# Optimization experiments

Hardware: AMD Instinct MI355X
Metric: run time of the kernel (lower is better)

Reference implementation:

```python
import jax, jax.numpy as jnp
import numpy as np
from jax import lax

NI, NH, NO = 128, 64, 128
PERIODS = np.array([1, 2, 4, 8, 16, 32, 64, 128], dtype=np.int32)
NCLOCKS = len(PERIODS)
K = NCLOCKS * NH  # total hidden size = 512
T, B = 512, 256


def _glorotize(W):
    W = W * np.sqrt(6.0)
    W = W / np.sqrt(np.sum(W.shape))
    return W


def _recurrent_mask():
    # block upper-triangular: row block r can read hidden blocks r..NCLOCKS-1
    rows = []
    for c in range(NCLOCKS, 0, -1):
        zero = np.zeros((NH, NH * (NCLOCKS - c)))
        one = np.ones((NH, NH * c))
        rows.append(np.concatenate([zero, one], axis=1))
    return np.concatenate(rows, axis=0)


def setup_inputs() -> dict:
    key = jax.random.key(0)
    kx = jax.random.fold_in(key, 0)
    rng = np.random.default_rng(0)
    X = jax.random.normal(kx, (T, B, NI), dtype=jnp.float32)
    Wi = _glorotize(rng.standard_normal((K, NI + 1)))
    Wh = rng.standard_normal((K, K + 1))
    U, _, _ = np.linalg.svd(Wh[:, :-1])
    Wh[:, :-1] = U * _recurrent_mask()
    Wo = _glorotize(rng.standard_normal((NO, K + 1)))
    return {
        "X": X,
        "Wi": jnp.asarray(Wi, jnp.float32),
        "Wh": jnp.asarray(Wh, jnp.float32),
        "Wo": jnp.asarray(Wo, jnp.float32),
    }


def reference(X, Wi, Wh, Wo):
    # X: (T, B, NI). Original code treats trailing axis as batch after transpose.
    periods = jnp.repeat(jnp.asarray(PERIODS), NH)               # (K,)
    active = ((jnp.arange(T)[:, None] % periods[None, :]) == 0)  # (T, K)
    active = active.astype(X.dtype)

    Xt = jnp.swapaxes(X, 1, 2)                                   # (T, NI, B)
    Wi_w, Wi_b = Wi[:, :-1], Wi[:, -1:]                          # (K,NI),(K,1)
    Wh_w, Wh_b = Wh[:, :-1], Wh[:, -1:]                          # (K,K),(K,1)
    Wo_w, Wo_b = Wo[:, :-1], Wo[:, -1:]                          # (NO,K),(NO,1)

    def step(H_prev, inp):
        x, a = inp                                               # (NI,B),(K,)
        i_h = Wi_w @ x + Wi_b                                    # (K,B)
        H_new = jnp.tanh(i_h + Wh_w @ H_prev + Wh_b)             # (K,B)
        a = a[:, None]
        H = a * H_new + (1.0 - a) * H_prev                       # clock gating
        y = jnp.tanh(Wo_w @ H + Wo_b)                            # (NO,B)
        return H, y

    H0 = jnp.zeros((K, B), dtype=X.dtype)
    H, Ys = lax.scan(step, H0, (Xt, active))                     # Ys: (T,NO,B)
    return jnp.swapaxes(Ys, 1, 2), H                             # (T,B,NO),(K,B)
```

## Files before the change

kernel.cpp:

```cpp
#include <hip/hip_runtime.h>


typedef unsigned int  u32;
typedef unsigned short u16;
typedef _Float16 f16;
typedef f16   f16x2 __attribute__((ext_vector_type(2)));
typedef f16   f16x8 __attribute__((ext_vector_type(8)));
typedef float f32x4 __attribute__((ext_vector_type(4)));

#define TT   512
#define BB   256
#define NI_  128
#define NO_  128

#define WIP_N   32768
#define WHRP_N  49152
#define WHLP_N  30720
#define WOA_N   32768
#define ICOMP_PER_B 65280
#define IOFF(j_) (65536 - (65536 >> (j_)))

__device__ __forceinline__ u32 pk2(float a, float b){
  f16x2 v; v.x=(f16)a; v.y=(f16)b; return __builtin_bit_cast(u32, v);
}
__device__ __forceinline__ float tanh_fast(float x){
  float e = __expf(2.0f*x);
  return 1.0f - 2.0f/(e + 1.0f);
}
__device__ __forceinline__ float dot2(u32 a, u32 b, float c){
#if __has_builtin(__builtin_amdgcn_fdot2)
  return __builtin_amdgcn_fdot2(__builtin_bit_cast(f16x2,a), __builtin_bit_cast(f16x2,b), c, false);
#else
  f16x2 x = __builtin_bit_cast(f16x2,a), y = __builtin_bit_cast(f16x2,b);
  c = fmaf((float)x.x,(float)y.x,c); c = fmaf((float)x.y,(float)y.y,c); return c;
#endif
}
__device__ __forceinline__ float f16at_rt(uint4 v, int i){
  u32 w = (i&4) ? ((i&2)? v.w : v.z) : ((i&2)? v.y : v.x);
  w = (i&1) ? (w>>16) : (w & 0xffffu);
  return (float)__builtin_bit_cast(f16, (u16)w);
}
__device__ __forceinline__ float f16at2(uint2 v, int i){
  u32 w = (i&2) ? v.y : v.x;
  w = (i&1) ? (w>>16) : (w & 0xffffu);
  return (float)__builtin_bit_cast(f16, (u16)w);
}
__device__ __forceinline__ float f16at1(u32 v, int i){
  u32 w = i ? (v>>16) : (v & 0xffffu);
  return (float)__builtin_bit_cast(f16, (u16)w);
}

#define BAR()   asm volatile("s_waitcnt lgkmcnt(0)\n\ts_barrier" ::: "memory")
#define LGKMW() do{ asm volatile("s_waitcnt lgkmcnt(0)" ::: "memory"); \
                    __builtin_amdgcn_sched_barrier(0); }while(0)

__global__ __launch_bounds__(256) void cw_prep(
    const float* __restrict__ Wi, const float* __restrict__ Wh, const float* __restrict__ Wo,
    u32* __restrict__ WiP, u32* __restrict__ WhrP, u32* __restrict__ WhlP, u32* __restrict__ WoAu,
    float* __restrict__ cb, float* __restrict__ wob)
{
  const int NTOT = WIP_N + WHRP_N + WHLP_N + WOA_N + 512 + 128;
  for (int idx = blockIdx.x*blockDim.x + threadIdx.x; idx < NTOT; idx += (int)(gridDim.x*blockDim.x)){
    if (idx < WIP_N){
      int r  = idx >> 6;
      int c2 = idx & 63;
      WiP[idx] = pk2(Wi[r*129 + 2*c2], Wi[r*129 + 2*c2 + 1]);
    } else if (idx < WIP_N + WHRP_N){
      int q32 = idx - WIP_N;
      int slot = q32 >> 11, rr = (q32 >> 5) & 63, c4 = q32 & 31;
      int jj = slot / 3, dq = slot % 3, qq = jj + dq;
      u32 v = 0u;
      if (qq <= 7){
        int row = 64*jj + rr;
        v = pk2(Wh[row*513 + 64*qq + 2*c4], Wh[row*513 + 64*qq + 2*c4 + 1]);
      }
      WhrP[q32] = v;
    } else if (idx < WIP_N + WHRP_N + WHLP_N){
      int q32 = idx - WIP_N - WHRP_N;
      int slot = q32 >> 11, rr = (q32 >> 5) & 63, pos = (q32 >> 2) & 7, e = q32 & 3;
      int jj, qq;
      if      (slot <  5){ jj = 0; qq = slot + 3; }
      else if (slot <  9){ jj = 1; qq = slot - 1; }
      else if (slot < 12){ jj = 2; qq = slot - 4; }
      else if (slot < 14){ jj = 3; qq = slot - 6; }
      else               { jj = 4; qq = 7; }
      int i  = pos ^ (rr & 7);
      int cp = i*4 + e;
      int row = 64*jj + rr;
      WhlP[q32] = pk2(Wh[row*513 + 64*qq + 2*cp], Wh[row*513 + 64*qq + 2*cp + 1]);
    } else if (idx < WIP_N + WHRP_N + WHLP_N + WOA_N){
      int q32 = idx - WIP_N - WHRP_N - WHLP_N;
      int o = q32 >> 8, kp = q32 & 255;
      WoAu[q32] = pk2(Wo[o*513 + 2*kp], Wo[o*513 + 2*kp + 1]);
    } else if (idx < WIP_N + WHRP_N + WHLP_N + WOA_N + 512){
      int r = idx - WIP_N - WHRP_N - WHLP_N - WOA_N;
      cb[r] = Wh[r*513 + 512] + Wi[r*129 + 128];
    } else {
      int o = idx - WIP_N - WHRP_N - WHLP_N - WOA_N - 512;
      wob[o] = Wo[o*513 + 512];
    }
  }
}

__global__ __launch_bounds__(256) void cw_igemm(
    const float* __restrict__ X, const u32* __restrict__ WiP, f16* __restrict__ Icomp)
{
  const int tid = threadIdx.x;
  const int l = tid & 63, w = tid >> 6;
  const int bid = blockIdx.x;
  const int b = bid / 19, sub = bid % 19;
  int j, m0;
  if      (sub <  8){ j = 0; m0 = sub*64; }
  else if (sub < 12){ j = 1; m0 = (sub-8)*64; }
  else if (sub < 14){ j = 2; m0 = (sub-12)*64; }
  else if (sub ==14){ j = 3; m0 = 0; }
  else              { j = sub-11; m0 = 0; }
  const int Nj = 512 >> j;
  const int mt = m0 + w*16;
  const int la = l & 15, lb = l >> 4;

  int ma = mt + la; if (ma >= Nj) ma = Nj - 1;
  const int t = ma << j;
  const float* Xr = X + ((size_t)t*BB + b)*NI_ + lb*8;
  const u32* wp0 = WiP + (j<<12) + la*64 + lb*4;

  f32x4 a0 = {0.f,0.f,0.f,0.f}, a1 = a0, a2 = a0, a3 = a0;
  #pragma unroll
  for (int ks = 0; ks < 4; ++ks){
    const float4 x0 = *(const float4*)(Xr + ks*32);
    const float4 x1 = *(const float4*)(Xr + ks*32 + 4);
    uint4 au;
    au.x = __builtin_bit_cast(u32, __builtin_amdgcn_cvt_pkrtz(x0.x, x0.y));
    au.y = __builtin_bit_cast(u32, __builtin_amdgcn_cvt_pkrtz(x0.z, x0.w));
    au.z = __builtin_bit_cast(u32, __builtin_amdgcn_cvt_pkrtz(x1.x, x1.y));
    au.w = __builtin_bit_cast(u32, __builtin_amdgcn_cvt_pkrtz(x1.z, x1.w));
    const f16x8 af = __builtin_bit_cast(f16x8, au);
    const u32* wp = wp0 + ks*16;
    a0 = __builtin_amdgcn_mfma_f32_16x16x32_f16(af, __builtin_bit_cast(f16x8, *(const uint4*)(wp       )), a0, 0,0,0);
    a1 = __builtin_amdgcn_mfma_f32_16x16x32_f16(af, __builtin_bit_cast(f16x8, *(const uint4*)(wp + 1024)), a1, 0,0,0);
    a2 = __builtin_amdgcn_mfma_f32_16x16x32_f16(af, __builtin_bit_cast(f16x8, *(const uint4*)(wp + 2048)), a2, 0,0,0);
    a3 = __builtin_amdgcn_mfma_f32_16x16x32_f16(af, __builtin_bit_cast(f16x8, *(const uint4*)(wp + 3072)), a3, 0,0,0);
  }
  const int mb = mt + lb*4;
  if (mb < Nj){
    const size_t offj = 65536 - (65536 >> j);
    f16* base = Icomp + (size_t)b*ICOMP_PER_B + offj + mb;
    uint2 s;
    s.x = __builtin_bit_cast(u32, __builtin_amdgcn_cvt_pkrtz(a0[0], a0[1]));
    s.y = __builtin_bit_cast(u32, __builtin_amdgcn_cvt_pkrtz(a0[2], a0[3]));
    *(uint2*)(base + (size_t)( 0 + la)*Nj) = s;
    s.x = __builtin_bit_cast(u32, __builtin_amdgcn_cvt_pkrtz(a1[0], a1[1]));
    s.y = __builtin_bit_cast(u32, __builtin_amdgcn_cvt_pkrtz(a1[2], a1[3]));
    *(uint2*)(base + (size_t)(16 + la)*Nj) = s;
    s.x = __builtin_bit_cast(u32, __builtin_amdgcn_cvt_pkrtz(a2[0], a2[1]));
    s.y = __builtin_bit_cast(u32, __builtin_amdgcn_cvt_pkrtz(a2[2], a2[3]));
    *(uint2*)(base + (size_t)(32 + la)*Nj) = s;
    s.x = __builtin_bit_cast(u32, __builtin_amdgcn_cvt_pkrtz(a3[0], a3[1]));
    s.y = __builtin_bit_cast(u32, __builtin_amdgcn_cvt_pkrtz(a3[2], a3[3]));
    *(uint2*)(base + (size_t)(48 + la)*Nj) = s;
  }
}

__device__ __forceinline__ float gemv8(const uint4 (&W)[8], const u32* hq){
  float a0=0.f, a1=0.f, a2=0.f, a3=0.f;
  #pragma unroll
  for (int i = 0; i < 8; ++i){
    const uint4 hv = *(const uint4*)(hq + (i<<2));
    a0 = dot2(W[i].x, hv.x, a0); a1 = dot2(W[i].y, hv.y, a1);
    a2 = dot2(W[i].z, hv.z, a2); a3 = dot2(W[i].w, hv.w, a3);
  }
  return (a0+a1)+(a2+a3);
}
__device__ __forceinline__ float dotreg8(const uint4 (&W)[8], const uint4 (&H)[8]){
  float a0=0.f, a1=0.f, a2=0.f, a3=0.f;
  #pragma unroll
  for (int i = 0; i < 8; ++i){
    a0 = dot2(W[i].x, H[i].x, a0); a1 = dot2(W[i].y, H[i].y, a1);
    a2 = dot2(W[i].z, H[i].z, a2); a3 = dot2(W[i].w, H[i].w, a3);
  }
  return (a0+a1)+(a2+a3);
}
__device__ __forceinline__ float gemv_sw(const u32* __restrict__ wp, const u32* hq, int lx){
  float a0=0.f, a1=0.f, a2=0.f, a3=0.f;
  #pragma unroll
  for (int i = 0; i < 8; ++i){
    const uint4 w  = *(const uint4*)(wp + ((i ^ lx) << 2));
    const uint4 hv = *(const uint4*)(hq + (i<<2));
    a0 = dot2(w.x, hv.x, a0); a1 = dot2(w.y, hv.y, a1);
    a2 = dot2(w.z, hv.z, a2); a3 = dot2(w.w, hv.w, a3);
  }
  return (a0+a1)+(a2+a3);
}
__device__ __forceinline__ float gemv_ns(const u32* __restrict__ wp, const u32* hq){
  float a0=0.f, a1=0.f, a2=0.f, a3=0.f;
  #pragma unroll
  for (int i = 0; i < 8; ++i){
    const uint4 w  = *(const uint4*)(wp + (i << 2));
    const uint4 hv = *(const uint4*)(hq + (i<<2));
    a0 = dot2(w.x, hv.x, a0); a1 = dot2(w.y, hv.y, a1);
    a2 = dot2(w.z, hv.z, a2); a3 = dot2(w.w, hv.w, a3);
  }
  return (a0+a1)+(a2+a3);
}

#define SPR(hr_, q_, s_) ((const u32*)((hr_) + (((((q_)-3)*4) + (int)(s_)) << 6)))

template<int X>
__device__ __forceinline__ void helper_entries(int per, float* __restrict__ tabp,
    const u32* __restrict__ whr, const u32* __restrict__ whl,
    const u16* __restrict__ hring, int l)
{
  const int lx = l & 7;
  #pragma unroll
  for (int q = 3; q <= 7; ++q){
    if ((per & ((1 << (q-3)) - 1)) == 0){
      const u32 v = ((u32)(8*per) >> q) + 1;
      const u32* hq = SPR(hring, q, v & 3);
      float val;
      if constexpr (X == 0){
        val = gemv_sw(whl + (q-3)*2048 + l*32, hq, lx);
      } else {
        if (q == 3) val = gemv_ns(whr + 5*2048 + l*32, hq);
        else        val = gemv_sw(whl + (5 + (q-4))*2048 + l*32, hq, lx);
      }
      tabp[(X*5 + (q-3))*64 + l] = val;
    }
  }
}

template<int J>
__device__ void run_waveJ(const f16* __restrict__ Ib, const u32* __restrict__ whr,
                          const u32* __restrict__ whl, u16* hring,
                          f16* __restrict__ Hc, float* __restrict__ Hout,
                          float cbv, int r, int b)
{
  constexpr int NJ  = 512 >> J;
  constexpr int ND  = 8 - J;
  constexpr int TWJ = 1 << J;
  const int lx = r & 7;

  uint4 W0[8], W1[8], W2[8];
  {
    const u32* w0 = whr + (J*3)*2048 + r*32;
    #pragma unroll
    for (int i = 0; i < 8; ++i) W0[i] = *(const uint4*)(w0 + (i<<2));
    if constexpr (ND > 1){
      #pragma unroll
      for (int i = 0; i < 8; ++i) W1[i] = *(const uint4*)(w0 + 2048 + (i<<2));
    }
    if constexpr (ND > 2){
      #pragma unroll
      for (int i = 0; i < 8; ++i) W2[i] = *(const uint4*)(w0 + 4096 + (i<<2));
    }
  }
  float ctx[8];
  #pragma unroll
  for (int q = 0; q < 8; ++q) ctx[q] = 0.f;

  uint4 icur = {0,0,0,0}, inxt = {0,0,0,0};
  if constexpr (NJ >= 8) icur = *(const uint4*)(Ib);
  else { const uint2 u2 = *(const uint2*)(Ib); icur.x = u2.x; icur.y = u2.y; }
  if constexpr (NJ > 8) inxt = *(const uint4*)(Ib + 8);

  float h;
  {
    h = tanh_fast(cbv + f16at_rt(icur, 0));
    const f16 h16 = (f16)h;
    hring[(((J-3)*4 + 1) << 6) + r] = __builtin_bit_cast(u16, h16);
    Hc[r] = h16;
    LGKMW();
    ctx[J] = gemv8(W0, SPR(hring, J, 1));
  }

  auto body = [&](int t){
    if ((t & (TWJ - 1)) != 0) return;
    const int tm = t - TWJ;
    const int cc0 = (tm == 0) ? 7 : __builtin_ctz((u32)tm);
    const int cc = cc0 > 7 ? 7 : cc0;
    if constexpr (ND > 1){
      if (cc >= J + 1){ const u32 v = ((u32)tm >> (J + 1)) + 1;
        ctx[J+1] = gemv8(W1, SPR(hring, J+1, v & 3)); }
    }
    if constexpr (ND > 2){
      if (cc >= J + 2){ const u32 v = ((u32)tm >> (J + 2)) + 1;
        ctx[J+2] = gemv8(W2, SPR(hring, J+2, v & 3)); }
    }
    if constexpr (J == 3){
      if (cc >= 6){ const u32 v = ((u32)tm >> 6) + 1; ctx[6] = gemv_sw(whl + 12*2048 + r*32, SPR(hring, 6, v & 3), lx); }
      if (cc >= 7){ const u32 v = ((u32)tm >> 7) + 1; ctx[7] = gemv_sw(whl + 13*2048 + r*32, SPR(hring, 7, v & 3), lx); }
    }
    if constexpr (J == 4){
      if (cc >= 7){ const u32 v = ((u32)tm >> 7) + 1; ctx[7] = gemv_sw(whl + 14*2048 + r*32, SPR(hring, 7, v & 3), lx); }
    }
    const int m = t >> J, e = m & 7;
    if constexpr (NJ > 8){ if (e == 0 && m + 8 < NJ) inxt = *(const uint4*)(Ib + m + 8); }
    float z = cbv + f16at_rt(icur, e);
    #pragma unroll
    for (int q = J; q < 8; ++q) z += ctx[q];
    h = tanh_fast(z);
    const f16 h16 = (f16)h;
    const int sl = (m + 1) & 3;
    hring[(((J-3)*4 + sl) << 6) + r] = __builtin_bit_cast(u16, h16);
    Hc[(m << 6) + r] = h16;
    LGKMW();
    ctx[J] = gemv8(W0, SPR(hring, J, sl));
    if constexpr (NJ > 8){ if (e == 7) icur = inxt; }
  };

  BAR();
  body(8);
  BAR();
  for (int k = 0; k < 64; ++k){
    const int t = 8*(k + 2);
    if (t < 512) body(t);
    BAR();
  }
  Hout[(J*64 + r)*BB + b] = h;
}

__global__ __launch_bounds__(512) void cw_serial(
    const f16* __restrict__ Icomp, const u32* __restrict__ WhrP, const u32* __restrict__ WhlP,
    const float* __restrict__ cbg, f16* __restrict__ Hcomp, float* __restrict__ Hout)
{
  __shared__ u32 sW2[6144];
  __shared__ __align__(16) u16 hring[5*4*64];
  __shared__ __align__(16) u16 sh01[128];
  __shared__ __align__(16) u16 sh2[128];
  __shared__ float ctxTab[2*960];
  __shared__ float tab2[512];

  const int tid = (int)threadIdx.x;
  const int b   = (int)blockIdx.x;
  const int wv  = tid >> 6, l = tid & 63;

  for (int i = tid; i < 2048; i += 512){
    const int rr = i >> 5, c4 = i & 31, ch = c4 >> 2, e = c4 & 3;
    const int dst = rr*32 + (((ch ^ rr) & 7) << 2) + e;
    sW2[       dst] = WhrP[2*2048 + i];
    sW2[2048 + dst] = WhrP[4*2048 + i];
    sW2[4096 + dst] = WhrP[6*2048 + i];
  }
  __syncthreads();

  if (wv == 0 || wv == 2) __builtin_amdgcn_s_setprio(1);

  const f16* Ibase = Icomp + (size_t)b*ICOMP_PER_B;
  f16*       Hbase = Hcomp + (size_t)b*ICOMP_PER_B;

  if (wv == 0){
    u16* shw = sh01;
    const u32* shu = (const u32*)sh01;

    uint4 w00[8], w01[8], w11[8];
    #pragma unroll
    for (int i = 0; i < 8; ++i){
      w00[i] = *(const uint4*)(WhrP +      0 + l*32 + (i<<2));
      w01[i] = *(const uint4*)(WhrP +   2048 + l*32 + (i<<2));
      w11[i] = *(const uint4*)(WhrP + 3*2048 + l*32 + (i<<2));
    }
    const float cb0 = cbg[l], cb1 = cbg[64+l];
    float c00=0.f,c01=0.f,c11=0.f,c02=0.f,c12=0.f;
    float c3a[5]={0,0,0,0,0}, c3b[5]={0,0,0,0,0};
    float zq0=cb0, zq1=cb1;
    float h0v=0.f, h1v=0.f;

    const u16* Ib0 = (const u16*)Ibase + l*512;
    const u16* Ib1 = (const u16*)Ibase + 32768 + l*256;
    u16* Hb0 = (u16*)Hbase;
    u16* Hb1 = (u16*)Hbase + 32768;

    uint4 icur0 = *(const uint4*)(Ib0);
    uint2 icur1 = *(const uint2*)(Ib1);

    {
      h0v = tanh_fast(cb0 + f16at_rt(icur0, 0));
      h1v = tanh_fast(cb1 + f16at2(icur1, 0));
      const f16 a0=(f16)h0v, a1=(f16)h1v;
      shw[l]    = __builtin_bit_cast(u16,a0);
      shw[64+l] = __builtin_bit_cast(u16,a1);
      Hb0[l] = __builtin_bit_cast(u16,a0);
      Hb1[l] = __builtin_bit_cast(u16,a1);
      c00 = gemv8(w00, shu);
      uint4 hq1[8];
      #pragma unroll
      for (int i = 0; i < 8; ++i) hq1[i] = *(const uint4*)(shu + 32 + (i<<2));
      c01 = dotreg8(w01, hq1); c11 = dotreg8(w11, hq1);
    }
    BAR();
    BAR();

#define W0_STEP(S_, B1_) do{ \
      const int t_ = 8*k + (S_); \
      float z0 = zq0 + c01 + c02 + c00 + f16at_rt(icur0, (S_)); \
      float z1 = 0.f; \
      if (B1_) z1 = zq1 + c11 + c12 + f16at2(icur1, (S_)>>1); \
      h0v = tanh_fast(z0); \
      if (B1_) h1v = tanh_fast(z1); \
      { const f16 a=(f16)h0v; shw[l] = __builtin_bit_cast(u16,a); \
        Hb0[(t_<<6)+l] = __builtin_bit_cast(u16,a); } \
      if (B1_){ const f16 a=(f16)h1v; shw[64+l] = __builtin_bit_cast(u16,a); \
        Hb1[((4*k+((S_)>>1))<<6)+l] = __builtin_bit_cast(u16,a); } \
      c00 = gemv8(w00, shu); \
      if (B1_){ uint4 hq1[8]; \
        _Pragma("unroll") for (int i = 0; i < 8; ++i) hq1[i] = *(const uint4*)(shu + 32 + (i<<2)); \
        c01 = dotreg8(w01, hq1); c11 = dotreg8(w11, hq1); } \
    }while(0)

    for (int k = 0; k < 64; ++k){
      uint4 inxt0 = icur0; uint2 inxt1 = icur1;
      const bool pf = (k < 63);
      if (pf){
        inxt0 = *(const uint4*)(Ib0 + 8*(k+1));
        inxt1 = *(const uint2*)(Ib1 + 4*(k+1));
      }
      if (k > 0) W0_STEP(0, 1);
      {
        const float* tab = ctxTab + (k & 1)*960;
                { c3a[0]=tab[0*64+l]; c3b[0]=tab[5*64+l]; }
        if((k&1)==0)   { c3a[1]=tab[1*64+l]; c3b[1]=tab[6*64+l]; }
        if((k&3)==0)   { c3a[2]=tab[2*64+l]; c3b[2]=tab[7*64+l]; }
        if((k&7)==0)   { c3a[3]=tab[3*64+l]; c3b[3]=tab[8*64+l]; }
        if((k&15)==0)  { c3a[4]=tab[4*64+l]; c3b[4]=tab[9*64+l]; }
        zq0 = cb0 + (((c3a[0]+c3a[1])+(c3a[2]+c3a[3]))+c3a[4]);
        zq1 = cb1 + (((c3b[0]+c3b[1])+(c3b[2]+c3b[3]))+c3b[4]);
      }
      c02 = tab2[(k&1)*256 +   0 + l];
      c12 = tab2[(k&1)*256 +  64 + l];
      W0_STEP(1,0); W0_STEP(2,1); W0_STEP(3,0); W0_STEP(4,1);
      c02 = tab2[(k&1)*256 + 128 + l];
      c12 = tab2[(k&1)*256 + 192 + l];
      W0_STEP(5,0); W0_STEP(6,1); W0_STEP(7,0);
      if (pf){ icur0 = inxt0; icur1 = inxt1; }
      BAR();
    }
#undef W0_STEP
    Hout[l*BB + b]      = h0v;
    Hout[(64+l)*BB + b] = h1v;

  } else if (wv == 1){
    BAR();
    helper_entries<0>(0, ctxTab, WhrP, WhlP, hring, l);
    helper_entries<1>(0, ctxTab, WhrP, WhlP, hring, l);
    BAR();
    for (int k = 0; k < 64; ++k){
      const int per = k + 1;
      if (per < 64){
        float* tp = ctxTab + (per & 1)*960;
        helper_entries<0>(per, tp, WhrP, WhlP, hring, l);
        helper_entries<1>(per, tp, WhrP, WhlP, hring, l);
      }
      BAR();
    }
  } else if (wv == 2){
    const int lx = l & 7;
    uint4 W23r[8], W24r[8];
    #pragma unroll
    for (int i = 0; i < 8; ++i){
      W23r[i] = *(const uint4*)(WhrP + 7*2048 + l*32 + (i<<2));
      W24r[i] = *(const uint4*)(WhrP + 8*2048 + l*32 + (i<<2));
    }
    const float cb2 = cbg[128+l];
    float c22=0.f,c23=0.f,c24=0.f,c25=0.f,c26=0.f,c27=0.f;
    int vp3=0,vp4=0,vp5=0,vp6=0,vp7=0;
    const u16* Ib2 = (const u16*)Ibase + 49152 + l*128;
    u16* Hb2 = (u16*)Hbase + 49152;
    float h2v = 0.f;
    u32 icp = *(const u32*)(Ib2);

    {
      h2v = tanh_fast(cb2 + f16at1(icp, 0));
      const f16 a=(f16)h2v;
      sh2[l] = __builtin_bit_cast(u16,a);
      Hb2[l] = __builtin_bit_cast(u16,a);
      const u32* hb = (const u32*)sh2;
      tab2[  0 + l] = gemv_sw(sW2 +        l*32, hb, lx);
      tab2[ 64 + l] = gemv_sw(sW2 + 2048 + l*32, hb, lx);
    }
    BAR();
    {
      c23 = gemv8(W23r, SPR(hring, 3, 1)); vp3 = 1;
      c24 = gemv8(W24r, SPR(hring, 4, 1)); vp4 = 1;
      c25 = gemv_sw(WhlP +  9*2048 + l*32, SPR(hring, 5, 1), lx); vp5 = 1;
      c26 = gemv_sw(WhlP + 10*2048 + l*32, SPR(hring, 6, 1), lx); vp6 = 1;
      c27 = gemv_sw(WhlP + 11*2048 + l*32, SPR(hring, 7, 1), lx); vp7 = 1;
      c22 = gemv_sw(sW2 + 4096 + l*32, (const u32*)sh2, lx);
      float z2 = cb2 + f16at1(icp, 1) + ((c22 + c23) + (c24 + c25)) + (c26 + c27);
      h2v = tanh_fast(z2);
      const f16 a=(f16)h2v;
      sh2[64+l] = __builtin_bit_cast(u16,a);
      Hb2[64+l] = __builtin_bit_cast(u16,a);
      const u32* hb = (const u32*)(sh2 + 64);
      tab2[128 + l] = gemv_sw(sW2 +        l*32, hb, lx);
      tab2[192 + l] = gemv_sw(sW2 + 2048 + l*32, hb, lx);
    }
    BAR();

    for (int k = 0; k < 64; ++k){
      if (k <= 62){
        const int m1 = 2*(k+1);
        icp = *(const u32*)(Ib2 + m1);
        const int par = (k+1) & 1;
        {
          const int t = m1 << 2;
          { const int v = ((t-1)>>3)+1; if (v != vp3){ c23 = gemv8(W23r, SPR(hring,3,v&3)); vp3 = v; } }
          { const int v = ((t-1)>>4)+1; if (v != vp4){ c24 = gemv8(W24r, SPR(hring,4,v&3)); vp4 = v; } }
          { const int v = ((t-1)>>5)+1; if (v != vp5){ c25 = gemv_sw(WhlP +  9*2048 + l*32, SPR(hring,5,v&3), lx); vp5 = v; } }
          { const int v = ((t-1)>>6)+1; if (v != vp6){ c26 = gemv_sw(WhlP + 10*2048 + l*32, SPR(hring,6,v&3), lx); vp6 = v; } }
          { const int v = ((t-1)>>7)+1; if (v != vp7){ c27 = gemv_sw(WhlP + 11*2048 + l*32, SPR(hring,7,v&3), lx); vp7 = v; } }
          c22 = gemv_sw(sW2 + 4096 + l*32, (const u32*)(sh2 + 64), lx);
          float z2 = cb2 + f16at1(icp, 0) + ((c22 + c23) + (c24 + c25)) + (c26 + c27);
          h2v = tanh_fast(z2);
          const f16 a=(f16)h2v;
          sh2[l] = __builtin_bit_cast(u16,a);
          Hb2[(m1<<6)+l] = __builtin_bit_cast(u16,a);
          const u32* hb = (const u32*)sh2;
          tab2[par*256 +   0 + l] = gemv_sw(sW2 +        l*32, hb, lx);
          tab2[par*256 +  64 + l] = gemv_sw(sW2 + 2048 + l*32, hb, lx);
        }
        {
          const int t = (m1+1) << 2;
          { const int v = ((t-1)>>3)+1; if (v != vp3){ c23 = gemv8(W23r, SPR(hring,3,v&3)); vp3 = v; } }
          { const int v = ((t-1)>>4)+1; if (v != vp4){ c24 = gemv8(W24r, SPR(hring,4,v&3)); vp4 = v; } }
          { const int v = ((t-1)>>5)+1; if (v != vp5){ c25 = gemv_sw(WhlP +  9*2048 + l*32, SPR(hring,5,v&3), lx); vp5 = v; } }
          { const int v = ((t-1)>>6)+1; if (v != vp6){ c26 = gemv_sw(WhlP + 10*2048 + l*32, SPR(hring,6,v&3), lx); vp6 = v; } }
          { const int v = ((t-1)>>7)+1; if (v != vp7){ c27 = gemv_sw(WhlP + 11*2048 + l*32, SPR(hring,7,v&3), lx); vp7 = v; } }
          c22 = gemv_sw(sW2 + 4096 + l*32, (const u32*)sh2, lx);
          float z2 = cb2 + f16at1(icp, 1) + ((c22 + c23) + (c24 + c25)) + (c26 + c27);
          h2v = tanh_fast(z2);
          const f16 a=(f16)h2v;
          sh2[64+l] = __builtin_bit_cast(u16,a);
          Hb2[((m1+1)<<6)+l] = __builtin_bit_cast(u16,a);
          const u32* hb = (const u32*)(sh2 + 64);
          tab2[par*256 + 128 + l] = gemv_sw(sW2 +        l*32, hb, lx);
          tab2[par*256 + 192 + l] = gemv_sw(sW2 + 2048 + l*32, hb, lx);
        }
      }
      BAR();
    }
    Hout[(128+l)*BB + b] = h2v;

  } else {
    const int J = wv;
    const float cbv = cbg[J*64 + l];
    const f16* Ib = Ibase + IOFF(J) + l*(512 >> J);
    f16* Hc = Hbase + IOFF(J);
    switch (J){
      case 3: run_waveJ<3>(Ib, WhrP, WhlP, hring, Hc, Hout, cbv, l, b); break;
      case 4: run_waveJ<4>(Ib, WhrP, WhlP, hring, Hc, Hout, cbv, l, b); break;
      case 5: run_waveJ<5>(Ib, WhrP, WhlP, hring, Hc, Hout, cbv, l, b); break;
      case 6: run_waveJ<6>(Ib, WhrP, WhlP, hring, Hc, Hout, cbv, l, b); break;
      default: run_waveJ<7>(Ib, WhrP, WhlP, hring, Hc, Hout, cbv, l, b); break;
    }
  }
}

__global__ __launch_bounds__(512) void cw_ygemm4(
    const f16* __restrict__ Hcomp, const u32* __restrict__ WoAu,
    const float* __restrict__ wobg, float* __restrict__ Y)
{
  const int tid = (int)threadIdx.x;
  const int w = tid >> 6, l = tid & 63;
  const int la = l & 15, lb = l >> 4;
  const int b  = (int)blockIdx.x;
  const int op = (w & 3) * 2;
  const int t0 = (int)blockIdx.y * 128 + (w >> 2) * 64;

  uint4 A0[16], A1[16];
  {
    const u32* ap = WoAu + (op*16 + la)*256 + lb*4;
    #pragma unroll
    for (int ks = 0; ks < 16; ++ks){
      A0[ks] = *(const uint4*)(ap + ks*16);
      A1[ks] = *(const uint4*)(ap + 16*256 + ks*16);
    }
  }
  const float4 wv0 = *(const float4*)(wobg + op*16 + lb*4);
  const float4 wv1 = *(const float4*)(wobg + (op+1)*16 + lb*4);
  const f16* Hb = Hcomp + (size_t)b * ICOMP_PER_B;

  #pragma unroll
  for (int tt = 0; tt < 4; ++tt){
    const int tA = t0 + tt*16 + la;
    f32x4 ac0 = {0.f,0.f,0.f,0.f}, ac1 = ac0;
    #pragma unroll
    for (int ks = 0; ks < 16; ++ks){
      const int j   = ks >> 1;
      const int m   = tA >> j;
      const int off = IOFF(j) + (m << 6) + ((ks & 1) << 5) + lb*8;
      const f16x8 Bf = __builtin_bit_cast(f16x8, *(const uint4*)(Hb + off));
      ac0 = __builtin_amdgcn_mfma_f32_16x16x32_f16(__builtin_bit_cast(f16x8, A0[ks]), Bf, ac0, 0,0,0);
      ac1 = __builtin_amdgcn_mfma_f32_16x16x32_f16(__builtin_bit_cast(f16x8, A1[ks]), Bf, ac1, 0,0,0);
    }
    float* Yr = Y + ((size_t)(t0 + tt*16 + la)*BB + b)*NO_;
    float4 y0, y1;
    y0.x = tanh_fast(ac0[0] + wv0.x); y0.y = tanh_fast(ac0[1] + wv0.y);
    y0.z = tanh_fast(ac0[2] + wv0.z); y0.w = tanh_fast(ac0[3] + wv0.w);
    y1.x = tanh_fast(ac1[0] + wv1.x); y1.y = tanh_fast(ac1[1] + wv1.y);
    y1.z = tanh_fast(ac1[2] + wv1.z); y1.w = tanh_fast(ac1[3] + wv1.w);
    *(float4*)(Yr + op*16 + lb*4)       = y0;
    *(float4*)(Yr + (op+1)*16 + lb*4)   = y1;
  }
}

extern "C" void kernel_launch(void* const* d_in, const int* in_sizes, int n_in,
                              void* d_out, int out_size, void* d_ws, size_t ws_size,
                              hipStream_t stream)
{
  const float* X  = (const float*)d_in[0];
  const float* Wi = (const float*)d_in[1];
  const float* Wh = (const float*)d_in[2];
  const float* Wo = (const float*)d_in[3];

  u32*   WiP  = (u32*)d_ws;
  u32*   WhrP = WiP  + WIP_N;
  u32*   WhlP = WhrP + WHRP_N;
  u32*   WoAu = WhlP + WHLP_N;
  float* cb   = (float*)(WoAu + WOA_N);
  float* wob  = cb + 512;
  f16*   Icomp = (f16*)(wob + 128);
  f16*   Hcomp = Icomp + (size_t)BB * ICOMP_PER_B;

  float* Y    = (float*)d_out;
  float* Hout = Y + (size_t)TT*BB*NO_;

  const int prep_n = WIP_N + WHRP_N + WHLP_N + WOA_N + 512 + 128;
  hipLaunchKernelGGL(cw_prep, dim3((prep_n + 255)/256), dim3(256), 0, stream,
                     Wi, Wh, Wo, WiP, WhrP, WhlP, WoAu, cb, wob);

  hipLaunchKernelGGL(cw_igemm, dim3(256*19), dim3(256), 0, stream, X, WiP, Icomp);

  hipLaunchKernelGGL(cw_serial, dim3(BB), dim3(512), 0, stream,
                     Icomp, WhrP, WhlP, cb, Hcomp, Hout);

  hipLaunchKernelGGL(cw_ygemm4, dim3(BB, 4), dim3(512), 0, stream,
                     Hcomp, WoAu, wob, Y);
}
```

Measured before the change: 308.2 us.

## Stage per-batch hidden history in swizzled LDS for output GEMM

The output GEMM now runs one block per batch column instead of four. It first copies that batch's whole compressed hidden history (about 130KB) into LDS with an XOR swizzle, then loops over all 512 timesteps reading MFMA B fragments from LDS instead of global memory. This avoids re-reading the Wo A fragments in four blocks and replaces scattered global loads with bank-conflict-free LDS reads. The cost is a large LDS allocation that limits occupancy to one block per CU, fewer blocks in the grid, and an upfront serialized copy phase.

Result: faster. 283.3 us (-8.1%).

```diff
diff --git a/kernel.cpp b/kernel.cpp
--- a/kernel.cpp
+++ b/kernel.cpp
@@ -19,6 +19,8 @@
 #define WOA_N   32768
 #define ICOMP_PER_B 65280
 #define IOFF(j_) (65536 - (65536 >> (j_)))
+
+#define YG_LDS 130560
 
 __device__ __forceinline__ u32 pk2(float a, float b){
   f16x2 v; v.x=(f16)a; v.y=(f16)b; return __builtin_bit_cast(u32, v);
@@ -554,16 +556,28 @@
   }
 }
 
-__global__ __launch_bounds__(512) void cw_ygemm4(
+__global__ __launch_bounds__(512) void cw_ygemm5(
     const f16* __restrict__ Hcomp, const u32* __restrict__ WoAu,
     const float* __restrict__ wobg, float* __restrict__ Y)
 {
+  extern __shared__ u32 sH[];
   const int tid = (int)threadIdx.x;
   const int w = tid >> 6, l = tid & 63;
   const int la = l & 15, lb = l >> 4;
   const int b  = (int)blockIdx.x;
+
+  {
+    const uint4* src = (const uint4*)(Hcomp + (size_t)b*ICOMP_PER_B);
+    uint4* dst = (uint4*)sH;
+    for (int i = tid; i < 8160; i += 512){
+      const int row = i >> 3, c = i & 7;
+      dst[row*8 + (c ^ (row & 7))] = src[i];
+    }
+  }
+  __syncthreads();
+
   const int op = (w & 3) * 2;
-  const int t0 = (int)blockIdx.y * 128 + (w >> 2) * 64;
+  const int t0w = (w >> 2) * 256;
 
   uint4 A0[16], A1[16];
   {
@@ -576,29 +590,29 @@
   }
   const float4 wv0 = *(const float4*)(wobg + op*16 + lb*4);
   const float4 wv1 = *(const float4*)(wobg + (op+1)*16 + lb*4);
-  const f16* Hb = Hcomp + (size_t)b * ICOMP_PER_B;
-
-  #pragma unroll
-  for (int tt = 0; tt < 4; ++tt){
-    const int tA = t0 + tt*16 + la;
+
+  for (int tt = 0; tt < 16; ++tt){
+    const int tA = t0w + tt*16 + la;
     f32x4 ac0 = {0.f,0.f,0.f,0.f}, ac1 = ac0;
     #pragma unroll
     for (int ks = 0; ks < 16; ++ks){
-      const int j   = ks >> 1;
-      const int m   = tA >> j;
-      const int off = IOFF(j) + (m << 6) + ((ks & 1) << 5) + lb*8;
-      const f16x8 Bf = __builtin_bit_cast(f16x8, *(const uint4*)(Hb + off));
+      const int j     = ks >> 1;
+      const int m     = tA >> j;
+      const int row   = (IOFF(j) >> 6) + m;
+      const int chunk = ((ks & 1) << 2) + lb;
+      const uint4 Bu  = *(const uint4*)(sH + row*32 + ((chunk ^ (row & 7)) << 2));
+      const f16x8 Bf  = __builtin_bit_cast(f16x8, Bu);
       ac0 = __builtin_amdgcn_mfma_f32_16x16x32_f16(__builtin_bit_cast(f16x8, A0[ks]), Bf, ac0, 0,0,0);
       ac1 = __builtin_amdgcn_mfma_f32_16x16x32_f16(__builtin_bit_cast(f16x8, A1[ks]), Bf, ac1, 0,0,0);
     }
-    float* Yr = Y + ((size_t)(t0 + tt*16 + la)*BB + b)*NO_;
+    float* Yr = Y + ((size_t)tA*BB + b)*NO_;
     float4 y0, y1;
     y0.x = tanh_fast(ac0[0] + wv0.x); y0.y = tanh_fast(ac0[1] + wv0.y);
     y0.z = tanh_fast(ac0[2] + wv0.z); y0.w = tanh_fast(ac0[3] + wv0.w);
     y1.x = tanh_fast(ac1[0] + wv1.x); y1.y = tanh_fast(ac1[1] + wv1.y);
     y1.z = tanh_fast(ac1[2] + wv1.z); y1.w = tanh_fast(ac1[3] + wv1.w);
-    *(float4*)(Yr + op*16 + lb*4)       = y0;
-    *(float4*)(Yr + (op+1)*16 + lb*4)   = y1;
+    *(float4*)(Yr + op*16 + lb*4)     = y0;
+    *(float4*)(Yr + (op+1)*16 + lb*4) = y1;
   }
 }
 
@@ -632,6 +646,8 @@
   hipLaunchKernelGGL(cw_serial, dim3(BB), dim3(512), 0, stream,
                      Icomp, WhrP, WhlP, cb, Hcomp, Hout);
 
-  hipLaunchKernelGGL(cw_ygemm4, dim3(BB, 4), dim3(512), 0, stream,
+  hipFuncSetAttribute(reinterpret_cast<const void*>(cw_ygemm5),
+                      hipFuncAttributeMaxDynamicSharedMemorySize, YG_LDS);
+  hipLaunchKernelGGL(cw_ygemm5, dim3(BB), dim3(512), YG_LDS, stream,
                      Hcomp, WoAu, wob, Y);
 }
```
